# Performance work log

Hardware: AMD Instinct MI355X
Metric: run time of the kernel (lower is better)

The kernel has to match this reference:

```python
import jax, jax.numpy as jnp
import numpy as np

SAMPLE_RATE = 16000
WIN_LENGTH = 1024
N_HARMONICS = 64
HALF_BANDWIDTH = 1.0


def setup_inputs() -> dict:
    key = jax.random.key(0)
    k1, k2 = jax.random.split(key)
    B, T, C = 4, 200, 1
    audio_frames = jax.random.normal(k1, (B, T, C, WIN_LENGTH), dtype=jnp.float32)
    # realistic fundamental frequencies in [50, 500) Hz
    f0 = 50.0 + 450.0 * jax.random.uniform(k2, (B, T, C), dtype=jnp.float32)
    return {"audio_frames": audio_frames, "f0": f0}


def reference(audio_frames, f0):
    n = jnp.arange(WIN_LENGTH, dtype=jnp.float32)            # [N]
    k = jnp.arange(1, N_HARMONICS + 1, dtype=jnp.float32)    # [K]
    tp = (1.0 / HALF_BANDWIDTH) * SAMPLE_RATE

    # fc: normalized harmonic frequencies, [B,T,C,K]
    fc = jnp.einsum('btc,k->btck', f0, k) / SAMPLE_RATE
    # fc_n: phase argument, [B,T,C,K,N]
    fc_n = fc[..., None] * n

    normalizer = np.float32(1.0 / np.sqrt(np.pi * tp))
    gauss = jnp.exp(-((n - WIN_LENGTH // 2) ** 2) / tp)      # [N]
    wave = jnp.exp(-2j * np.pi * fc_n)                        # [B,T,C,K,N] complex64
    morlet = (normalizer * gauss) * wave
    # zero out harmonics above Nyquist (fc > 0.5)
    morlet = morlet * (fc <= 0.5)[..., None]

    transform = jnp.einsum('btckn,btcn->btck', morlet,
                           audio_frames.astype(jnp.complex64))
    transform = jnp.abs(transform)                            # [B,T,C,K]
    amp = jnp.sum(transform, axis=-1, keepdims=True)          # [B,T,C,1]
    harmonic_distribution = transform / amp
    amp = jnp.clip(amp * 2.0, 0.0, 1.0).squeeze(-1)           # [B,T,C]
    return harmonic_distribution, amp
```

## Files before the change

kernel.cpp:

```cpp
#include <hip/hip_runtime.h>
#include <math.h>

#define WIN 1024
#define NH 64
#define PAD 16

__global__ __launch_bounds__(256) void morlet_goertzel(
    const float* __restrict__ x,
    const float* __restrict__ f0,
    float* __restrict__ hd,
    float* __restrict__ amp)
{
    const int frame = blockIdx.x;
    const int tid   = threadIdx.x;
    const int lane  = tid & 63;
    const int wave  = tid >> 6;

    __shared__ float y[WIN + PAD];
    __shared__ float pr[4][NH];
    __shared__ float pi_[4][NH];

    const float f0v = f0[frame];

    {
        const float4 v =
            reinterpret_cast<const float4*>(x + (size_t)frame * WIN)[tid];
        const float inv_tp = 1.0f / 16000.0f;
        const float norm   = 0.0044603129f;
        const int n0 = 4 * tid;
        const float d0 = (float)(n0 - 512);
        const float d1 = d0 + 1.0f;
        const float d2 = d0 + 2.0f;
        const float d3 = d0 + 3.0f;
        y[n0 + 0] = v.x * (norm * __expf(-d0 * d0 * inv_tp));
        y[n0 + 1] = v.y * (norm * __expf(-d1 * d1 * inv_tp));
        y[n0 + 2] = v.z * (norm * __expf(-d2 * d2 * inv_tp));
        y[n0 + 3] = v.w * (norm * __expf(-d3 * d3 * inv_tp));
        if (tid < PAD) y[WIN + tid] = 0.0f;
    }
    __syncthreads();

    const float fc = f0v * (float)(lane + 1) * (1.0f / 16000.0f);
    const float tw = fc - floorf(fc);
    const float c1  = __builtin_amdgcn_cosf(tw);
    const float sn1 = __builtin_amdgcn_sinf(tw);
    const float coef = 2.0f * c1;

    float a1 = 0.0f, a2 = 0.0f, b1 = 0.0f, b2 = 0.0f;

#define GSTEP(ch1, ch2, yv) { const float t_ = fmaf(coef, ch1, (yv) - ch2); ch2 = ch1; ch1 = t_; }

    const int base = 256 * wave;
    float4 A0 = *(const float4*)&y[base];
    float4 A1 = *(const float4*)&y[base + 4];
    float4 B0 = *(const float4*)&y[base + 128];
    float4 B1 = *(const float4*)&y[base + 132];

    #pragma unroll 4
    for (int i = 0; i < 128; i += 8) {
        const float4 nA0 = *(const float4*)&y[base + i + 8];
        const float4 nA1 = *(const float4*)&y[base + i + 12];
        const float4 nB0 = *(const float4*)&y[base + 128 + i + 8];
        const float4 nB1 = *(const float4*)&y[base + 128 + i + 12];
        GSTEP(a1, a2, A0.x) GSTEP(a1, a2, A0.y) GSTEP(a1, a2, A0.z) GSTEP(a1, a2, A0.w)
        GSTEP(a1, a2, A1.x) GSTEP(a1, a2, A1.y) GSTEP(a1, a2, A1.z) GSTEP(a1, a2, A1.w)
        GSTEP(b1, b2, B0.x) GSTEP(b1, b2, B0.y) GSTEP(b1, b2, B0.z) GSTEP(b1, b2, B0.w)
        GSTEP(b1, b2, B1.x) GSTEP(b1, b2, B1.y) GSTEP(b1, b2, B1.z) GSTEP(b1, b2, B1.w)
        A0 = nA0; A1 = nA1; B0 = nB0; B1 = nB1;
    }
#undef GSTEP

    const int qA = 2 * wave, qB = 2 * wave + 1;
    float tA = fc * (float)(128 * qA + 127); tA -= floorf(tA);
    float tB = fc * (float)(128 * qB + 127); tB -= floorf(tB);
    const float cA = __builtin_amdgcn_cosf(tA), sA = __builtin_amdgcn_sinf(tA);
    const float cB = __builtin_amdgcn_cosf(tB), sB = __builtin_amdgcn_sinf(tB);

    const float urA = fmaf(-c1, a2, a1);
    const float uiA = sn1 * a2;
    const float urB = fmaf(-c1, b2, b1);
    const float uiB = sn1 * b2;

    const float reW = fmaf(cA, urA,  sA * uiA) + fmaf(cB, urB,  sB * uiB);
    const float imW = fmaf(cA, uiA, -sA * urA) + fmaf(cB, uiB, -sB * urB);

    pr[wave][lane]  = reW;
    pi_[wave][lane] = imW;
    __syncthreads();

    if (tid < NH) {
        const float re = pr[0][tid] + pr[1][tid] + pr[2][tid] + pr[3][tid];
        const float im = pi_[0][tid] + pi_[1][tid] + pi_[2][tid] + pi_[3][tid];
        const float fck = f0v * (float)(tid + 1) * (1.0f / 16000.0f);
        const float v = (fck <= 0.5f) ? sqrtf(fmaf(re, re, im * im)) : 0.0f;
        float s = v;
        #pragma unroll
        for (int off = 32; off > 0; off >>= 1) s += __shfl_xor(s, off, 64);
        hd[(size_t)frame * NH + tid] = v / s;
        if (tid == 0) amp[frame] = fminf(fmaxf(s * 2.0f, 0.0f), 1.0f);
    }
}

extern "C" void kernel_launch(void* const* d_in, const int* in_sizes, int n_in,
                              void* d_out, int out_size, void* d_ws, size_t ws_size,
                              hipStream_t stream) {
    const float* x   = (const float*)d_in[0];
    const float* f0  = (const float*)d_in[1];
    const int F = in_sizes[1];
    float* hd  = (float*)d_out;
    float* amp = (float*)d_out + (size_t)F * NH;
    morlet_goertzel<<<F, 256, 0, stream>>>(x, f0, hd, amp);
}
```

Measured before the change: 60.30 us.

## Assign harmonic groups per wave and skip waves above Nyquist

Work is remapped so each wave owns 16 harmonics while its four 16-lane groups each take one quarter of the window. Partial sums are combined with cross-lane shuffles instead of shared-memory partial arrays. A wave whose lowest harmonic is already above Nyquist skips the Goertzel loop and writes zeros. The shared buffer gains padding of 4 floats after every 256 samples so the four lane groups read from different LDS banks. This trades a uniform workload for early exit at high f0, which cuts ALU work in frames with large f0.

Result: no change. 59.86 us (-0.7%).

```diff
diff --git a/kernel.cpp b/kernel.cpp
--- a/kernel.cpp
+++ b/kernel.cpp
@@ -3,7 +3,7 @@
 
 #define WIN 1024
 #define NH 64
-#define PAD 16
+#define YSZ 1056
 
 __global__ __launch_bounds__(256) void morlet_goertzel(
     const float* __restrict__ x,
@@ -16,9 +16,8 @@
     const int lane  = tid & 63;
     const int wave  = tid >> 6;
 
-    __shared__ float y[WIN + PAD];
-    __shared__ float pr[4][NH];
-    __shared__ float pi_[4][NH];
+    __shared__ float y[YSZ];
+    __shared__ float mag[NH];
 
     const float f0v = f0[frame];
 
@@ -28,71 +27,83 @@
         const float inv_tp = 1.0f / 16000.0f;
         const float norm   = 0.0044603129f;
         const int n0 = 4 * tid;
+        const int p0 = n0 + ((n0 >> 8) << 2);
         const float d0 = (float)(n0 - 512);
         const float d1 = d0 + 1.0f;
         const float d2 = d0 + 2.0f;
         const float d3 = d0 + 3.0f;
-        y[n0 + 0] = v.x * (norm * __expf(-d0 * d0 * inv_tp));
-        y[n0 + 1] = v.y * (norm * __expf(-d1 * d1 * inv_tp));
-        y[n0 + 2] = v.z * (norm * __expf(-d2 * d2 * inv_tp));
-        y[n0 + 3] = v.w * (norm * __expf(-d3 * d3 * inv_tp));
-        if (tid < PAD) y[WIN + tid] = 0.0f;
+        y[p0 + 0] = v.x * (norm * __expf(-d0 * d0 * inv_tp));
+        y[p0 + 1] = v.y * (norm * __expf(-d1 * d1 * inv_tp));
+        y[p0 + 2] = v.z * (norm * __expf(-d2 * d2 * inv_tp));
+        y[p0 + 3] = v.w * (norm * __expf(-d3 * d3 * inv_tp));
+        if (tid < 4) { y[256 + tid] = 0.0f; y[516 + tid] = 0.0f; y[776 + tid] = 0.0f; }
+        if (tid < YSZ - 1036) y[1036 + tid] = 0.0f;
     }
     __syncthreads();
 
-    const float fc = f0v * (float)(lane + 1) * (1.0f / 16000.0f);
-    const float tw = fc - floorf(fc);
-    const float c1  = __builtin_amdgcn_cosf(tw);
-    const float sn1 = __builtin_amdgcn_sinf(tw);
-    const float coef = 2.0f * c1;
+    const bool active = (f0v * (float)(16 * wave + 1) <= 8000.0f);
 
-    float a1 = 0.0f, a2 = 0.0f, b1 = 0.0f, b2 = 0.0f;
+    if (active) {
+        const int c = lane >> 4;
+        const int h = lane & 15;
+        const int k = 16 * wave + h + 1;
+        const float fc = f0v * (float)k * (1.0f / 16000.0f);
+        const float tw = fc - floorf(fc);
+        const float c1  = __builtin_amdgcn_cosf(tw);
+        const float sn1 = __builtin_amdgcn_sinf(tw);
+        const float coef = 2.0f * c1;
+
+        float a1 = 0.0f, a2 = 0.0f, b1 = 0.0f, b2 = 0.0f;
 
 #define GSTEP(ch1, ch2, yv) { const float t_ = fmaf(coef, ch1, (yv) - ch2); ch2 = ch1; ch1 = t_; }
 
-    const int base = 256 * wave;
-    float4 A0 = *(const float4*)&y[base];
-    float4 A1 = *(const float4*)&y[base + 4];
-    float4 B0 = *(const float4*)&y[base + 128];
-    float4 B1 = *(const float4*)&y[base + 132];
+        const int base = 260 * c;
+        float4 A0 = *(const float4*)&y[base];
+        float4 A1 = *(const float4*)&y[base + 4];
+        float4 B0 = *(const float4*)&y[base + 128];
+        float4 B1 = *(const float4*)&y[base + 132];
 
-    #pragma unroll 4
-    for (int i = 0; i < 128; i += 8) {
-        const float4 nA0 = *(const float4*)&y[base + i + 8];
-        const float4 nA1 = *(const float4*)&y[base + i + 12];
-        const float4 nB0 = *(const float4*)&y[base + 128 + i + 8];
-        const float4 nB1 = *(const float4*)&y[base + 128 + i + 12];
-        GSTEP(a1, a2, A0.x) GSTEP(a1, a2, A0.y) GSTEP(a1, a2, A0.z) GSTEP(a1, a2, A0.w)
-        GSTEP(a1, a2, A1.x) GSTEP(a1, a2, A1.y) GSTEP(a1, a2, A1.z) GSTEP(a1, a2, A1.w)
-        GSTEP(b1, b2, B0.x) GSTEP(b1, b2, B0.y) GSTEP(b1, b2, B0.z) GSTEP(b1, b2, B0.w)
-        GSTEP(b1, b2, B1.x) GSTEP(b1, b2, B1.y) GSTEP(b1, b2, B1.z) GSTEP(b1, b2, B1.w)
-        A0 = nA0; A1 = nA1; B0 = nB0; B1 = nB1;
-    }
+        #pragma unroll 4
+        for (int i = 0; i < 128; i += 8) {
+            const float4 nA0 = *(const float4*)&y[base + i + 8];
+            const float4 nA1 = *(const float4*)&y[base + i + 12];
+            const float4 nB0 = *(const float4*)&y[base + 128 + i + 8];
+            const float4 nB1 = *(const float4*)&y[base + 128 + i + 12];
+            GSTEP(a1, a2, A0.x) GSTEP(a1, a2, A0.y) GSTEP(a1, a2, A0.z) GSTEP(a1, a2, A0.w)
+            GSTEP(a1, a2, A1.x) GSTEP(a1, a2, A1.y) GSTEP(a1, a2, A1.z) GSTEP(a1, a2, A1.w)
+            GSTEP(b1, b2, B0.x) GSTEP(b1, b2, B0.y) GSTEP(b1, b2, B0.z) GSTEP(b1, b2, B0.w)
+            GSTEP(b1, b2, B1.x) GSTEP(b1, b2, B1.y) GSTEP(b1, b2, B1.z) GSTEP(b1, b2, B1.w)
+            A0 = nA0; A1 = nA1; B0 = nB0; B1 = nB1;
+        }
 #undef GSTEP
 
-    const int qA = 2 * wave, qB = 2 * wave + 1;
-    float tA = fc * (float)(128 * qA + 127); tA -= floorf(tA);
-    float tB = fc * (float)(128 * qB + 127); tB -= floorf(tB);
-    const float cA = __builtin_amdgcn_cosf(tA), sA = __builtin_amdgcn_sinf(tA);
-    const float cB = __builtin_amdgcn_cosf(tB), sB = __builtin_amdgcn_sinf(tB);
+        float tA = fc * (float)(256 * c + 127); tA -= floorf(tA);
+        float tB = fc * (float)(256 * c + 255); tB -= floorf(tB);
+        const float cA = __builtin_amdgcn_cosf(tA), sA = __builtin_amdgcn_sinf(tA);
+        const float cB = __builtin_amdgcn_cosf(tB), sB = __builtin_amdgcn_sinf(tB);
 
-    const float urA = fmaf(-c1, a2, a1);
-    const float uiA = sn1 * a2;
-    const float urB = fmaf(-c1, b2, b1);
-    const float uiB = sn1 * b2;
+        const float urA = fmaf(-c1, a2, a1);
+        const float uiA = sn1 * a2;
+        const float urB = fmaf(-c1, b2, b1);
+        const float uiB = sn1 * b2;
 
-    const float reW = fmaf(cA, urA,  sA * uiA) + fmaf(cB, urB,  sB * uiB);
-    const float imW = fmaf(cA, uiA, -sA * urA) + fmaf(cB, uiB, -sB * urB);
+        float reW = fmaf(cA, urA,  sA * uiA) + fmaf(cB, urB,  sB * uiB);
+        float imW = fmaf(cA, uiA, -sA * urA) + fmaf(cB, uiB, -sB * urB);
 
-    pr[wave][lane]  = reW;
-    pi_[wave][lane] = imW;
+        reW += __shfl_xor(reW, 16, 64);  imW += __shfl_xor(imW, 16, 64);
+        reW += __shfl_xor(reW, 32, 64);  imW += __shfl_xor(imW, 32, 64);
+
+        if (lane < 16) {
+            const float v = (fc <= 0.5f) ? sqrtf(fmaf(reW, reW, imW * imW)) : 0.0f;
+            mag[16 * wave + lane] = v;
+        }
+    } else if (lane < 16) {
+        mag[16 * wave + lane] = 0.0f;
+    }
     __syncthreads();
 
     if (tid < NH) {
-        const float re = pr[0][tid] + pr[1][tid] + pr[2][tid] + pr[3][tid];
-        const float im = pi_[0][tid] + pi_[1][tid] + pi_[2][tid] + pi_[3][tid];
-        const float fck = f0v * (float)(tid + 1) * (1.0f / 16000.0f);
-        const float v = (fck <= 0.5f) ? sqrtf(fmaf(re, re, im * im)) : 0.0f;
+        const float v = mag[tid];
         float s = v;
         #pragma unroll
         for (int off = 32; off > 0; off >>= 1) s += __shfl_xor(s, off, 64);
```
